# Kernel optimization log

Measured on AMD Instinct MI355X. Metric: run time of the kernel, lower is better.

Reference implementation:

```python
import jax, jax.numpy as jnp
import numpy as np

BS, SL = 32, 2048
N_VALUES, N_KEYS = 256, 256
VOCAB = N_VALUES + N_KEYS
D, E, NU = 256, 256, 2  # dpfp -> phi dim p = 2*NU*D = 1024
EPS = 1e-6


def dpfp(x, nu):
    # deterministic-parameter-free-projection feature map
    x = jnp.concatenate([jax.nn.relu(x), jax.nn.relu(-x)], axis=-1)  # [..., 2d]
    rolled = jnp.concatenate([jnp.roll(x, j, axis=-1) for j in range(1, nu + 1)], axis=-1)
    repeated = jnp.concatenate([x] * nu, axis=-1)
    return repeated * rolled  # [..., 2*nu*d]


def setup_inputs() -> dict:
    key = jax.random.key(0)
    k1, k2, k3, k4, k5, k6, k7, k8 = jax.random.split(key, 8)
    key_idx = jax.random.randint(k1, (BS, SL), 0, VOCAB)
    val_idx = jax.random.randint(k2, (BS, SL), N_VALUES, VOCAB)  # in-range for '- n_values'
    x = jnp.stack([key_idx, val_idx], axis=1)  # [BS, 2, SL]
    q = jax.random.randint(k3, (BS, 1), 0, VOCAB)
    embK = jax.random.normal(k4, (VOCAB, E), dtype=jnp.float32)  # std=1 init
    u = 1.0 / np.sqrt(D)
    Wk_w = jax.random.uniform(k5, (D, E + N_VALUES), minval=-u, maxval=u, dtype=jnp.float32)
    Wk_b = jax.random.uniform(k6, (D,), minval=-u, maxval=u, dtype=jnp.float32)
    Wq_w = jax.random.uniform(k7, (D, E), minval=-u, maxval=u, dtype=jnp.float32)
    Wq_b = jax.random.uniform(k8, (D,), minval=-u, maxval=u, dtype=jnp.float32)
    return {"x": x, "q": q, "embK": embK, "Wk_w": Wk_w, "Wk_b": Wk_b,
            "Wq_w": Wq_w, "Wq_b": Wq_b}


def reference(x, q, embK, Wk_w, Wk_b, Wq_w, Wq_b):
    key_idx = x[:, 0, :]   # [BS, SL]
    val_idx = x[:, 1, :]   # [BS, SL]
    # embeddingV is fixed identity -> one-hot; computed under no_grad in original
    v_emb = jax.nn.one_hot(val_idx - N_VALUES, N_VALUES, dtype=embK.dtype)  # [BS,SL,NV]
    k_emb = embK[key_idx]                                                   # [BS,SL,E]
    xc = jnp.concatenate([v_emb, k_emb], axis=-1)                           # [BS,SL,E+NV]
    q_emb = embK[q]                                                         # [BS,1,E]

    K = xc @ Wk_w.T + Wk_b      # [BS,SL,D]
    Q = q_emb @ Wq_w.T + Wq_b   # [BS,1,D]

    K = dpfp(K, NU)             # [BS,SL,P]
    Q = dpfp(Q, NU)             # [BS,1,P]

    V = v_emb                   # [BS,SL,NV]
    VK = jnp.einsum('blv,blp->bvp', V, K)   # sum of K-V outer products
    Z = K.sum(axis=1)                        # [BS,P]

    num = jnp.einsum('bvp,blp->blv', VK, Q)                 # [BS,1,NV]
    den = jnp.einsum('bp,blp->bl', Z, Q)[..., None] + EPS   # [BS,1,1]
    y_hat = (num / den)[:, 0, :]                             # [BS,NV]
    return y_hat
```

## Files before the change

kernel.cpp:

```cpp
#include <hip/hip_runtime.h>

#define BSZ 32
#define SLEN 2048
#define NVAL 256
#define CHUNK 32
#define NCHUNK (SLEN / CHUNK)

__global__ __launch_bounds__(256) void k_pre(const int* __restrict__ q,
                                             const float* __restrict__ embK,
                                             const float* __restrict__ Wk_w,
                                             const float* __restrict__ Wk_b,
                                             const float* __restrict__ Wq_w,
                                             const float* __restrict__ Wq_b,
                                             float* __restrict__ Wv,
                                             float* __restrict__ Tb,
                                             float* __restrict__ Qp) {
  __shared__ float smem[64 * 65];
  int bx = blockIdx.x, tid = threadIdx.x;

  if (bx < 16) {
    float (*tile)[65] = (float(*)[65])smem;
    int c0 = (bx & 3) * 64, d0 = (bx >> 2) * 64;
    int tx = tid & 63, ty = tid >> 6;
#pragma unroll
    for (int j = 0; j < 16; ++j) {
      int dd = ty + j * 4;
      tile[dd][tx] = Wk_w[(d0 + dd) * 512 + c0 + tx];
    }
    __syncthreads();
#pragma unroll
    for (int j = 0; j < 16; ++j) {
      int cc = ty + j * 4;
      Wv[(c0 + cc) * 256 + d0 + tx] = tile[tx][cc];
    }
  } else if (bx < 80) {
    int k0 = (bx - 16) * 8;
    float* emb = smem;
#pragma unroll
    for (int t = 0; t < 8; ++t) emb[t * 256 + tid] = embK[(k0 + t) * 256 + tid];
    __syncthreads();
    float acc[8] = {0.f, 0.f, 0.f, 0.f, 0.f, 0.f, 0.f, 0.f};
    const float* wr = Wk_w + tid * 512 + 256;
    for (int e4 = 0; e4 < 64; ++e4) {
      float4 wv = *(const float4*)(wr + e4 * 4);
      const float wvf[4] = {wv.x, wv.y, wv.z, wv.w};
#pragma unroll
      for (int jj = 0; jj < 4; ++jj) {
        float we = wvf[jj];
        int e = e4 * 4 + jj;
#pragma unroll
        for (int k = 0; k < 8; ++k) acc[k] += we * emb[k * 256 + e];
      }
    }
    float bias = Wk_b[tid];
#pragma unroll
    for (int k = 0; k < 8; ++k) Tb[(k0 + k) * 256 + tid] = acc[k] + bias;
  } else {
    int b = bx - 80;
    float* qe = smem;
    float* xq = smem + 256;
    qe[tid] = embK[q[b] * 256 + tid];
    __syncthreads();
    float acc = Wq_b[tid];
    const float* wr = Wq_w + tid * 256;
    for (int e4 = 0; e4 < 64; ++e4) {
      float4 wv = *(const float4*)(wr + e4 * 4);
      int e = e4 * 4;
      acc += wv.x * qe[e] + wv.y * qe[e + 1] + wv.z * qe[e + 2] + wv.w * qe[e + 3];
    }
    xq[tid] = fmaxf(acc, 0.f);
    xq[tid + 256] = fmaxf(-acc, 0.f);
    __syncthreads();
#pragma unroll
    for (int t = 0; t < 4; ++t) {
      int p = tid + t * 256;
      float v = (p < 512) ? xq[p] * xq[(p - 1) & 511]
                          : xq[p - 512] * xq[(p - 514) & 511];
      Qp[b * 1024 + p] = v;
    }
  }
}

__global__ __launch_bounds__(256) void k_main(const int* __restrict__ x,
                                              const float* __restrict__ Wv,
                                              const float* __restrict__ Tb,
                                              const float* __restrict__ Qp,
                                              float* __restrict__ numP) {
  __shared__ float numW[4][256];
  __shared__ int kidx[CHUNK], vidx[CHUNK];
  int tid = threadIdx.x;
  int lane = tid & 63, w = tid >> 6;
  int b = blockIdx.x / NCHUNK, chunk = blockIdx.x % NCHUNK;
  int l0 = chunk * CHUNK;
  const int* xb = x + b * 2 * SLEN;

  if (tid < CHUNK) kidx[tid] = xb[l0 + tid];
  else if (tid < 2 * CHUNK) vidx[tid - CHUNK] = xb[SLEN + l0 + tid - CHUNK];
#pragma unroll
  for (int t = 0; t < 4; ++t) ((float*)numW)[tid + t * 256] = 0.f;
  __syncthreads();

  const float* Qb = Qp + b * 1024 + 4 * lane;
  float4 qa = *(const float4*)(Qb);
  float4 qc = *(const float4*)(Qb + 256);
  float4 qb4 = *(const float4*)(Qb + 512);
  float4 qd = *(const float4*)(Qb + 768);
  const float QA[4] = {qa.x, qa.y, qa.z, qa.w};
  const float QC[4] = {qc.x, qc.y, qc.z, qc.w};
  const float QB[4] = {qb4.x, qb4.y, qb4.z, qb4.w};
  const float QD[4] = {qd.x, qd.y, qd.z, qd.w};

  int src = (lane + 63) & 63;
  bool l0lane = (lane == 0);

  for (int p8 = 0; p8 < CHUNK / 4; ++p8) {
    int l = w + p8 * 4;
    int key = kidx[l];
    int vcol = vidx[l] - NVAL;
    float4 wv = *(const float4*)(Wv + vcol * 256 + 4 * lane);
    float4 tv = *(const float4*)(Tb + key * 256 + 4 * lane);
    float y[4] = {wv.x + tv.x, wv.y + tv.y, wv.z + tv.z, wv.w + tv.w};
    float xp0[4], xp1[4];
#pragma unroll
    for (int j = 0; j < 4; ++j) {
      xp0[j] = fmaxf(y[j], 0.f);
      xp1[j] = fmaxf(-y[j], 0.f);
    }
    float p0_3 = __shfl(xp0[3], src, 64);
    float p0_2 = __shfl(xp0[2], src, 64);
    float p1_3 = __shfl(xp1[3], src, 64);
    float p1_2 = __shfl(xp1[2], src, 64);
    float h0p1 = l0lane ? p1_3 : p0_3;
    float h0p2 = l0lane ? p1_2 : p0_2;
    float h1p1 = l0lane ? p0_3 : p1_3;
    float h1p2 = l0lane ? p0_2 : p1_2;

    float s = xp0[0] * (h0p1 * QA[0] + h0p2 * QB[0])
            + xp0[1] * (xp0[0] * QA[1] + h0p1 * QB[1])
            + xp0[2] * (xp0[1] * QA[2] + xp0[0] * QB[2])
            + xp0[3] * (xp0[2] * QA[3] + xp0[1] * QB[3])
            + xp1[0] * (h1p1 * QC[0] + h1p2 * QD[0])
            + xp1[1] * (xp1[0] * QC[1] + h1p1 * QD[1])
            + xp1[2] * (xp1[1] * QC[2] + xp1[0] * QD[2])
            + xp1[3] * (xp1[2] * QC[3] + xp1[1] * QD[3]);
#pragma unroll
    for (int off = 32; off >= 1; off >>= 1) s += __shfl_xor(s, off, 64);
    if (lane == 0) numW[w][vcol] += s;
  }
  __syncthreads();
  float tsum = numW[0][tid] + numW[1][tid] + numW[2][tid] + numW[3][tid];
  numP[(b * NCHUNK + chunk) * 256 + tid] = tsum;
}

__global__ __launch_bounds__(256) void k_final(const float* __restrict__ numP,
                                               float* __restrict__ out) {
  __shared__ float red[256];
  int b = blockIdx.x, v = threadIdx.x;
  float acc = 0.f;
  const float* p = numP + b * NCHUNK * 256 + v;
  for (int c = 0; c < NCHUNK; ++c) acc += p[c * 256];
  red[v] = acc;
  __syncthreads();
  if (v < 128) red[v] += red[v + 128];
  __syncthreads();
  if (v < 64) {
    float r = red[v] + red[v + 64];
#pragma unroll
    for (int off = 32; off >= 1; off >>= 1) r += __shfl_xor(r, off, 64);
    if (v == 0) red[0] = r;
  }
  __syncthreads();
  out[b * 256 + v] = acc / (red[0] + 1e-6f);
}

extern "C" void kernel_launch(void* const* d_in, const int* in_sizes, int n_in,
                              void* d_out, int out_size, void* d_ws, size_t ws_size,
                              hipStream_t stream) {
  const int* x = (const int*)d_in[0];
  const int* q = (const int*)d_in[1];
  const float* embK = (const float*)d_in[2];
  const float* Wk_w = (const float*)d_in[3];
  const float* Wk_b = (const float*)d_in[4];
  const float* Wq_w = (const float*)d_in[5];
  const float* Wq_b = (const float*)d_in[6];
  float* out = (float*)d_out;

  char* ws = (char*)d_ws;
  float* Wv   = (float*)ws; ws += 256 * 256 * 4;
  float* Tb   = (float*)ws; ws += 512 * 256 * 4;
  float* Qp   = (float*)ws; ws += 32 * 1024 * 4;
  float* numP = (float*)ws; ws += 32 * NCHUNK * 256 * 4;

  dim3 blk(256);
  k_pre<<<112, blk, 0, stream>>>(q, embK, Wk_w, Wk_b, Wq_w, Wq_b, Wv, Tb, Qp);
  k_main<<<BSZ * NCHUNK, blk, 0, stream>>>(x, Wv, Tb, Qp, numP);
  k_final<<<BSZ, blk, 0, stream>>>(numP, out);
}
```

Baseline: 92.39 us.

## Fuse final reduction into main kernel via last-block counter; widen Tb precompute grid

Removes the separate k_final launch: each k_main block bumps a per-batch atomic counter after writing its partial sums, and the last block for that batch performs the cross-chunk reduction and normalisation. The Tb precompute is split across 256 blocks of two rows each, reading embeddings directly from global memory instead of staging eight rows in shared memory, to spread the weight-dot work over more CUs. The counter is reset inside k_pre, which adds atomics and thread fences and depends on stream ordering between the two launches.

Result: slower. 240.4 us (+160.2%).

```diff
diff --git a/kernel.cpp b/kernel.cpp
--- a/kernel.cpp
+++ b/kernel.cpp
@@ -14,9 +14,12 @@
                                              const float* __restrict__ Wq_b,
                                              float* __restrict__ Wv,
                                              float* __restrict__ Tb,
-                                             float* __restrict__ Qp) {
+                                             float* __restrict__ Qp,
+                                             int* __restrict__ cnt) {
   __shared__ float smem[64 * 65];
   int bx = blockIdx.x, tid = threadIdx.x;
+
+  if (bx == 0 && tid < BSZ) cnt[tid] = 0;
 
   if (bx < 16) {
     float (*tile)[65] = (float(*)[65])smem;
@@ -33,40 +36,32 @@
       int cc = ty + j * 4;
       Wv[(c0 + cc) * 256 + d0 + tx] = tile[tx][cc];
     }
-  } else if (bx < 80) {
-    int k0 = (bx - 16) * 8;
-    float* emb = smem;
-#pragma unroll
-    for (int t = 0; t < 8; ++t) emb[t * 256 + tid] = embK[(k0 + t) * 256 + tid];
-    __syncthreads();
-    float acc[8] = {0.f, 0.f, 0.f, 0.f, 0.f, 0.f, 0.f, 0.f};
+  } else if (bx < 272) {
+    int k0 = (bx - 16) * 2;
+    const float* e0p = embK + k0 * 256;
+    const float* e1p = e0p + 256;
     const float* wr = Wk_w + tid * 512 + 256;
+    float acc0 = 0.f, acc1 = 0.f;
     for (int e4 = 0; e4 < 64; ++e4) {
       float4 wv = *(const float4*)(wr + e4 * 4);
-      const float wvf[4] = {wv.x, wv.y, wv.z, wv.w};
-#pragma unroll
-      for (int jj = 0; jj < 4; ++jj) {
-        float we = wvf[jj];
-        int e = e4 * 4 + jj;
-#pragma unroll
-        for (int k = 0; k < 8; ++k) acc[k] += we * emb[k * 256 + e];
-      }
+      float4 a = *(const float4*)(e0p + e4 * 4);
+      float4 c = *(const float4*)(e1p + e4 * 4);
+      acc0 += wv.x * a.x + wv.y * a.y + wv.z * a.z + wv.w * a.w;
+      acc1 += wv.x * c.x + wv.y * c.y + wv.z * c.z + wv.w * c.w;
     }
     float bias = Wk_b[tid];
-#pragma unroll
-    for (int k = 0; k < 8; ++k) Tb[(k0 + k) * 256 + tid] = acc[k] + bias;
+    Tb[k0 * 256 + tid] = acc0 + bias;
+    Tb[(k0 + 1) * 256 + tid] = acc1 + bias;
   } else {
-    int b = bx - 80;
-    float* qe = smem;
-    float* xq = smem + 256;
-    qe[tid] = embK[q[b] * 256 + tid];
-    __syncthreads();
+    int b = bx - 272;
+    float* xq = smem;
+    const float* qe = embK + q[b] * 256;
+    const float* wr = Wq_w + tid * 256;
     float acc = Wq_b[tid];
-    const float* wr = Wq_w + tid * 256;
     for (int e4 = 0; e4 < 64; ++e4) {
       float4 wv = *(const float4*)(wr + e4 * 4);
-      int e = e4 * 4;
-      acc += wv.x * qe[e] + wv.y * qe[e + 1] + wv.z * qe[e + 2] + wv.w * qe[e + 3];
+      float4 qv = *(const float4*)(qe + e4 * 4);
+      acc += wv.x * qv.x + wv.y * qv.y + wv.z * qv.z + wv.w * qv.w;
     }
     xq[tid] = fmaxf(acc, 0.f);
     xq[tid + 256] = fmaxf(-acc, 0.f);
@@ -85,9 +80,13 @@
                                               const float* __restrict__ Wv,
                                               const float* __restrict__ Tb,
                                               const float* __restrict__ Qp,
-                                              float* __restrict__ numP) {
+                                              float* __restrict__ numP,
+                                              int* __restrict__ cnt,
+                                              float* __restrict__ out) {
   __shared__ float numW[4][256];
+  __shared__ float red[256];
   __shared__ int kidx[CHUNK], vidx[CHUNK];
+  __shared__ int isLast;
   int tid = threadIdx.x;
   int lane = tid & 63, w = tid >> 6;
   int b = blockIdx.x / NCHUNK, chunk = blockIdx.x % NCHUNK;
@@ -150,27 +149,31 @@
   __syncthreads();
   float tsum = numW[0][tid] + numW[1][tid] + numW[2][tid] + numW[3][tid];
   numP[(b * NCHUNK + chunk) * 256 + tid] = tsum;
-}
-
-__global__ __launch_bounds__(256) void k_final(const float* __restrict__ numP,
-                                               float* __restrict__ out) {
-  __shared__ float red[256];
-  int b = blockIdx.x, v = threadIdx.x;
+
+  __threadfence();
+  if (tid == 0) {
+    int old = atomicAdd(&cnt[b], 1);
+    isLast = (old == NCHUNK - 1);
+  }
+  __syncthreads();
+  if (!isLast) return;
+  __threadfence();
+
   float acc = 0.f;
-  const float* p = numP + b * NCHUNK * 256 + v;
+  const float* p = numP + b * NCHUNK * 256 + tid;
   for (int c = 0; c < NCHUNK; ++c) acc += p[c * 256];
-  red[v] = acc;
-  __syncthreads();
-  if (v < 128) red[v] += red[v + 128];
-  __syncthreads();
-  if (v < 64) {
-    float r = red[v] + red[v + 64];
+  red[tid] = acc;
+  __syncthreads();
+  if (tid < 128) red[tid] += red[tid + 128];
+  __syncthreads();
+  if (tid < 64) {
+    float r = red[tid] + red[tid + 64];
 #pragma unroll
     for (int off = 32; off >= 1; off >>= 1) r += __shfl_xor(r, off, 64);
-    if (v == 0) red[0] = r;
-  }
-  __syncthreads();
-  out[b * 256 + v] = acc / (red[0] + 1e-6f);
+    if (tid == 0) red[0] = r;
+  }
+  __syncthreads();
+  out[b * 256 + tid] = acc / (red[0] + 1e-6f);
 }
 
 extern "C" void kernel_launch(void* const* d_in, const int* in_sizes, int n_in,
@@ -190,9 +193,9 @@
   float* Tb   = (float*)ws; ws += 512 * 256 * 4;
   float* Qp   = (float*)ws; ws += 32 * 1024 * 4;
   float* numP = (float*)ws; ws += 32 * NCHUNK * 256 * 4;
+  int*   cnt  = (int*)ws;   ws += 32 * 4;
 
   dim3 blk(256);
-  k_pre<<<112, blk, 0, stream>>>(q, embK, Wk_w, Wk_b, Wq_w, Wq_b, Wv, Tb, Qp);
-  k_main<<<BSZ * NCHUNK, blk, 0, stream>>>(x, Wv, Tb, Qp, numP);
-  k_final<<<BSZ, blk, 0, stream>>>(numP, out);
+  k_pre<<<304, blk, 0, stream>>>(q, embK, Wk_w, Wk_b, Wq_w, Wq_b, Wv, Tb, Qp, cnt);
+  k_main<<<BSZ * NCHUNK, blk, 0, stream>>>(x, Wv, Tb, Qp, numP, cnt, out);
 }
```
